# Performance work log

Hardware: AMD Instinct MI355X
Metric: run time of the kernel (lower is better)

Reference implementation:

```python
import jax, jax.numpy as jnp
import numpy as np

V, D, H, L, T, B = 50257, 768, 12, 12, 1024, 2
S = 0.02


def setup_inputs() -> dict:
    key = jax.random.key(0)
    ks = jax.random.split(key, 8)
    return {
        "idx": jax.random.randint(ks[0], (B, T), 0, V),
        "wte": jax.random.normal(ks[1], (V, D), jnp.float32) * S,   # tied tok_emb / head
        "pos": jax.random.normal(ks[2], (T, D), jnp.float32) * S,
        "ln1_g": jnp.ones((L, D), jnp.float32),
        "ln1_b": jnp.zeros((L, D), jnp.float32),
        "qkv_w": jax.random.normal(ks[3], (L, D, 3 * D), jnp.float32) * S,
        "qkv_b": jnp.zeros((L, 3 * D), jnp.float32),
        "proj_w": jax.random.normal(ks[4], (L, D, D), jnp.float32) * S,
        "proj_b": jnp.zeros((L, D), jnp.float32),
        "ln2_g": jnp.ones((L, D), jnp.float32),
        "ln2_b": jnp.zeros((L, D), jnp.float32),
        "fc1_w": jax.random.normal(ks[5], (L, D, 4 * D), jnp.float32) * S,
        "fc1_b": jnp.zeros((L, 4 * D), jnp.float32),
        "fc2_w": jax.random.normal(ks[6], (L, 4 * D, D), jnp.float32) * S,
        "fc2_b": jnp.zeros((L, D), jnp.float32),
        "lnf_g": jnp.ones((D,), jnp.float32),
        "lnf_b": jnp.zeros((D,), jnp.float32),
    }


def _ln(x, g, b):
    m = x.mean(-1, keepdims=True)
    v = ((x - m) ** 2).mean(-1, keepdims=True)
    return (x - m) * jax.lax.rsqrt(v + 1e-5) * g + b


def reference(idx, wte, pos, ln1_g, ln1_b, qkv_w, qkv_b, proj_w, proj_b,
              ln2_g, ln2_b, fc1_w, fc1_b, fc2_w, fc2_b, lnf_g, lnf_b):
    b, t = idx.shape
    hd = D // H
    x = wte[idx] + pos[None, :t]                       # [B,T,D]
    causal = jnp.triu(jnp.ones((t, t), bool), 1)       # True above diagonal -> masked

    def block(x, p):
        l1g, l1b, qw, qb, pw, pb, l2g, l2b, f1w, f1b, f2w, f2b = p
        h = _ln(x, l1g, l1b)
        qkv = (h @ qw + qb).reshape(b, t, 3, H, hd).transpose(2, 0, 3, 1, 4)
        q, k, v = qkv[0], qkv[1], qkv[2]               # [B,H,T,hd]
        att = jnp.einsum('bhqd,bhkd->bhqk', q, k) * hd ** -0.5
        att = jnp.where(causal, -jnp.inf, att)
        att = jax.nn.softmax(att, axis=-1)
        o = jnp.einsum('bhqk,bhkd->bhqd', att, v)
        o = o.transpose(0, 2, 1, 3).reshape(b, t, D)
        x = x + o @ pw + pb
        h = _ln(x, l2g, l2b)
        h = jax.nn.gelu(h @ f1w + f1b, approximate=False)
        x = x + h @ f2w + f2b
        return x, None

    x, _ = jax.lax.scan(block, x, (ln1_g, ln1_b, qkv_w, qkv_b, proj_w, proj_b,
                                   ln2_g, ln2_b, fc1_w, fc1_b, fc2_w, fc2_b))
    x = _ln(x, lnf_g, lnf_b)
    return x @ wte.T                                   # tied head -> [B,T,V]
```

## Files before the change

### kernel.cpp

```cpp
#include <hip/hip_runtime.h>
#include <math.h>

#define D 768
#define T 1024
#define BATCH 2
#define NH 12
#define NL 12
#define V 50257
#define NT 2048

typedef _Float16 half4_t __attribute__((ext_vector_type(4)));
typedef _Float16 half8_t __attribute__((ext_vector_type(8)));
typedef float floatx4 __attribute__((ext_vector_type(4)));

__device__ inline float wave_reduce_sum(float v) {
  #pragma unroll
  for (int off = 32; off > 0; off >>= 1) v += __shfl_xor(v, off, 64);
  return v;
}

__device__ __forceinline__ void gld16(const _Float16* g, _Float16* l) {
  __builtin_amdgcn_global_load_lds(
      (const __attribute__((address_space(1))) unsigned int*)g,
      (__attribute__((address_space(3))) unsigned int*)l, 16, 0, 0);
}

__global__ __launch_bounds__(256) void embed_kernel(const int* __restrict__ idx,
    const float* __restrict__ wte, const float* __restrict__ pos,
    float* __restrict__ x) {
  int row = blockIdx.x;
  int tok = idx[row];
  int tp  = row & (T - 1);
  const float* ws = wte + (size_t)tok * D;
  const float* ps = pos + (size_t)tp * D;
  float* xr = x + (size_t)row * D;
  for (int i = threadIdx.x; i < D; i += 256) xr[i] = ws[i] + ps[i];
}

__global__ __launch_bounds__(256) void cvt16_kernel(const float* __restrict__ src,
    _Float16* __restrict__ dst, int n4) {
  int i = blockIdx.x * 256 + threadIdx.x;
  int stride = gridDim.x * 256;
  for (; i < n4; i += stride) {
    float4 v = ((const float4*)src)[i];
    half4_t h;
    h[0] = (_Float16)v.x; h[1] = (_Float16)v.y;
    h[2] = (_Float16)v.z; h[3] = (_Float16)v.w;
    ((half4_t*)dst)[i] = h;
  }
}

__global__ __launch_bounds__(256) void wconv_kernel(
    const float* __restrict__ qkvw, const float* __restrict__ projw,
    const float* __restrict__ fc1w, const float* __restrict__ fc2w,
    _Float16* __restrict__ q16, _Float16* __restrict__ p16,
    _Float16* __restrict__ f116, _Float16* __restrict__ f216) {
  int id = blockIdx.x;
  size_t l = blockIdx.y;
  const float* src; _Float16* dst; int K, N, tn;
  if (id < 1728)      { src = qkvw + l * (D * 3 * D); dst = q16  + l * (2304 * 768); K = 768;  N = 2304; tn = id; }
  else if (id < 2304) { src = projw + l * (D * D);    dst = p16  + l * (768 * 768);  K = 768;  N = 768;  tn = id - 1728; }
  else if (id < 4608) { src = fc1w + l * (D * 4 * D); dst = f116 + l * (3072 * 768); K = 768;  N = 3072; tn = id - 2304; }
  else                { src = fc2w + l * (4 * D * D); dst = f216 + l * (3072 * 768); K = 3072; N = 768;  tn = id - 4608; }
  int ntn = N >> 5;
  int tc = (tn % ntn) * 32;
  int tr = (tn / ntn) * 32;
  __shared__ float tile[32][33];
  int tx = threadIdx.x & 31, ty = threadIdx.x >> 5;
  #pragma unroll
  for (int j = 0; j < 4; ++j)
    tile[ty + 8 * j][tx] = src[(size_t)(tr + ty + 8 * j) * N + tc + tx];
  __syncthreads();
  #pragma unroll
  for (int j = 0; j < 4; ++j)
    dst[(size_t)(tc + ty + 8 * j) * K + tr + tx] = (_Float16)tile[tx][ty + 8 * j];
}

__global__ __launch_bounds__(256) void ln_kernel(const float* __restrict__ x,
    const float* __restrict__ g, const float* __restrict__ bta,
    _Float16* __restrict__ y) {
  const int lane = threadIdx.x & 63, wave = threadIdx.x >> 6;
  const int row = blockIdx.x * 4 + wave;
  const float4* xr = (const float4*)(x + (size_t)row * D);
  half4_t* yr = (half4_t*)(y + (size_t)row * D);

  float4 a[3];
  #pragma unroll
  for (int j = 0; j < 3; ++j) a[j] = xr[lane + 64 * j];

  float s = 0.f;
  #pragma unroll
  for (int j = 0; j < 3; ++j) s += a[j].x + a[j].y + a[j].z + a[j].w;
  float mean = wave_reduce_sum(s) * (1.f / D);

  float v = 0.f;
  #pragma unroll
  for (int j = 0; j < 3; ++j) {
    float dx = a[j].x - mean, dy = a[j].y - mean, dz = a[j].z - mean, dw = a[j].w - mean;
    v += dx * dx + dy * dy + dz * dz + dw * dw;
  }
  float rstd = rsqrtf(wave_reduce_sum(v) * (1.f / D) + 1e-5f);

  #pragma unroll
  for (int j = 0; j < 3; ++j) {
    float4 gg = ((const float4*)g)[lane + 64 * j];
    float4 bb = ((const float4*)bta)[lane + 64 * j];
    half4_t h;
    h[0] = (_Float16)((a[j].x - mean) * rstd * gg.x + bb.x);
    h[1] = (_Float16)((a[j].y - mean) * rstd * gg.y + bb.y);
    h[2] = (_Float16)((a[j].z - mean) * rstd * gg.z + bb.z);
    h[3] = (_Float16)((a[j].w - mean) * rstd * gg.w + bb.w);
    yr[lane + 64 * j] = h;
  }
}

__global__ __launch_bounds__(256) void attn_kernel(
    const _Float16* __restrict__ qkv,
    const _Float16* __restrict__ vt,
    _Float16* __restrict__ o) {
  const int qt   = (int)gridDim.x - 1 - (int)blockIdx.x;
  const int h    = blockIdx.y;
  const int b    = blockIdx.z;
  const int tid  = threadIdx.x;
  const int lane = tid & 63, wave = tid >> 6;
  const int lr = lane & 15, g = lane >> 4;
  const int lk = g * 8;
  const int cr = g * 4;

  __shared__ __align__(16) _Float16 Ks[2][64][32];
  __shared__ __align__(16) _Float16 Vs[2][64][32];
  __shared__ __align__(16) _Float16 Pl[4][16][72];

  const int RS = 3 * D;
  const int q0 = qt * 64 + wave * 16;

  const _Float16* qrow = qkv + (size_t)(b * T + q0 + lr) * RS + h * 64;
  half8_t aq0 = *(const half8_t*)(qrow + lk);
  half8_t aq1 = *(const half8_t*)(qrow + 32 + lk);
  #pragma unroll
  for (int j = 0; j < 8; ++j) { aq0[j] *= (_Float16)0.125f; aq1[j] *= (_Float16)0.125f; }

  const int sr = wave * 16 + (lane >> 2);
  const int sc = (lane & 3) * 8;
  const _Float16* ksrc = qkv + (size_t)(b * T + sr) * RS + D + h * 64 + sc;
  const _Float16* vsrc = vt + (size_t)((b * NH + h) * 64 + sr) * T + sc;
  _Float16* kdst0 = &Ks[0][wave * 16][0];
  _Float16* kdst1 = &Ks[1][wave * 16][0];
  _Float16* vdst0 = &Vs[0][wave * 16][0];
  _Float16* vdst1 = &Vs[1][wave * 16][0];

  floatx4 oa[4] = {};
  float m_r[4] = {-1e30f, -1e30f, -1e30f, -1e30f};
  float l_r[4] = {0.f, 0.f, 0.f, 0.f};

  for (int kt = 0; kt <= qt; ++kt) {
    const _Float16* kp = ksrc + (size_t)(kt * 64) * RS;
    gld16(kp, kdst0);
    gld16(kp + 32, kdst1);
    gld16(vsrc + kt * 64, vdst0);
    gld16(vsrc + kt * 64 + 32, vdst1);
    __syncthreads();

    floatx4 s4[4];
    #pragma unroll
    for (int kc = 0; kc < 4; ++kc) {
      half8_t bk0 = *(const half8_t*)&Ks[0][kc * 16 + lr][lk];
      half8_t bk1 = *(const half8_t*)&Ks[1][kc * 16 + lr][lk];
      floatx4 z = {};
      z = __builtin_amdgcn_mfma_f32_16x16x32_f16(aq0, bk0, z, 0, 0, 0);
      z = __builtin_amdgcn_mfma_f32_16x16x32_f16(aq1, bk1, z, 0, 0, 0);
      s4[kc] = z;
    }
    if (kt == qt) {
      #pragma unroll
      for (int kc = 0; kc < 4; ++kc)
        #pragma unroll
        for (int i = 0; i < 4; ++i)
          if (kc * 16 + lr > wave * 16 + cr + i) s4[kc][i] = -1e30f;
    }

    float alpha[4], psum[4];
    #pragma unroll
    for (int i = 0; i < 4; ++i) {
      float v = fmaxf(fmaxf(s4[0][i], s4[1][i]), fmaxf(s4[2][i], s4[3][i]));
      #pragma unroll
      for (int off = 1; off < 16; off <<= 1) v = fmaxf(v, __shfl_xor(v, off, 64));
      float mn = fmaxf(m_r[i], v);
      alpha[i] = __expf(m_r[i] - mn);
      m_r[i] = mn;
      psum[i] = 0.f;
    }
    #pragma unroll
    for (int kc = 0; kc < 4; ++kc)
      #pragma unroll
      for (int i = 0; i < 4; ++i) {
        float p = __expf(s4[kc][i] - m_r[i]);
        psum[i] += p;
        Pl[wave][cr + i][kc * 16 + lr] = (_Float16)p;
      }
    #pragma unroll
    for (int i = 0; i < 4; ++i) {
      float s = psum[i];
      #pragma unroll
      for (int off = 1; off < 16; off <<= 1) s += __shfl_xor(s, off, 64);
      l_r[i] = l_r[i] * alpha[i] + s;
    }
    #pragma unroll
    for (int dc = 0; dc < 4; ++dc)
      #pragma unroll
      for (int i = 0; i < 4; ++i) oa[dc][i] *= alpha[i];

    half8_t ap0 = *(const half8_t*)&Pl[wave][lr][lk];
    half8_t ap1 = *(const half8_t*)&Pl[wave][lr][32 + lk];
    #pragma unroll
    for (int dc = 0; dc < 4; ++dc) {
      half8_t bv0 = *(const half8_t*)&Vs[0][dc * 16 + lr][lk];
      half8_t bv1 = *(const half8_t*)&Vs[1][dc * 16 + lr][lk];
      oa[dc] = __builtin_amdgcn_mfma_f32_16x16x32_f16(ap0, bv0, oa[dc], 0, 0, 0);
      oa[dc] = __builtin_amdgcn_mfma_f32_16x16x32_f16(ap1, bv1, oa[dc], 0, 0, 0);
    }
    __syncthreads();
  }

  _Float16* orow = o + (size_t)(b * T + q0) * D + h * 64;
  #pragma unroll
  for (int i = 0; i < 4; ++i) {
    float inv = 1.f / l_r[i];
    #pragma unroll
    for (int dc = 0; dc < 4; ++dc)
      orow[(size_t)(cr + i) * D + dc * 16 + lr] = (_Float16)(oa[dc][i] * inv);
  }
}

template <bool GELU, bool VT, bool ATOMIC, typename OutT>
__global__ __launch_bounds__(256) void gemm16_kernel(
    const _Float16* __restrict__ A, const _Float16* __restrict__ Bt,
    const float* __restrict__ bias, const float* __restrict__ res,
    OutT* __restrict__ C, _Float16* __restrict__ vt, int M, int N, int K) {
  __shared__ __align__(16) _Float16 As[128][32];
  __shared__ __align__(16) _Float16 Bs[128][32];
  const int t = threadIdx.x;
  const int lane = t & 63, wave = t >> 6;

  const int gx = gridDim.x, gy = gridDim.y;
  const int nwg = gx * gy;
  int f = blockIdx.y * gx + blockIdx.x;
  int id = (f & 7) * (nwg >> 3) + (f >> 3);
  const int n0 = (id / gy) * 128;
  const int m0 = (id % gy) * 128;

  const int ks = K / gridDim.z;
  const int kbeg = blockIdx.z * ks, kend = kbeg + ks;

  const int wm = (wave >> 1) * 64, wn = (wave & 1) * 64;
  const int lr = lane & 15;
  const int lk = (lane >> 4) * 8;

  const int srow = lane >> 2;
  const int scol = (lane & 3) * 8;
  const _Float16* a_src0 = A + (size_t)(m0 + wave * 32 + srow) * K + scol;
  const _Float16* a_src1 = a_src0 + (size_t)16 * K;
  const int bn0 = min(n0 + wave * 32 + srow, N - 1);
  const int bn1 = min(n0 + wave * 32 + 16 + srow, N - 1);
  const _Float16* b_src0 = Bt + (size_t)bn0 * K + scol;
  const _Float16* b_src1 = Bt + (size_t)bn1 * K + scol;
  _Float16* a_dst0 = &As[wave * 32][0];
  _Float16* a_dst1 = &As[wave * 32 + 16][0];
  _Float16* b_dst0 = &Bs[wave * 32][0];
  _Float16* b_dst1 = &Bs[wave * 32 + 16][0];

  floatx4 acc[4][4] = {};

  for (int k0 = kbeg; k0 < kend; k0 += 32) {
    gld16(a_src0 + k0, a_dst0);
    gld16(a_src1 + k0, a_dst1);
    gld16(b_src0 + k0, b_dst0);
    gld16(b_src1 + k0, b_dst1);
    __syncthreads();

    half8_t af[4], bf[4];
    #pragma unroll
    for (int mi = 0; mi < 4; ++mi)
      af[mi] = *(const half8_t*)&As[wm + mi * 16 + lr][lk];
    #pragma unroll
    for (int ni = 0; ni < 4; ++ni)
      bf[ni] = *(const half8_t*)&Bs[wn + ni * 16 + lr][lk];
    #pragma unroll
    for (int mi = 0; mi < 4; ++mi)
      #pragma unroll
      for (int ni = 0; ni < 4; ++ni)
        acc[mi][ni] = __builtin_amdgcn_mfma_f32_16x16x32_f16(
            af[mi], bf[ni], acc[mi][ni], 0, 0, 0);
    __syncthreads();
  }

  const int cr = (lane >> 4) * 4;
  #pragma unroll
  for (int mi = 0; mi < 4; ++mi) {
    #pragma unroll
    for (int ni = 0; ni < 4; ++ni) {
      int n = n0 + wn + ni * 16 + lr;
      if (n >= N) continue;
      floatx4 v = acc[mi][ni];
      float bs = (bias && (!ATOMIC || blockIdx.z == 0)) ? bias[n] : 0.f;
      if (VT && n >= 2 * D) {
        int d  = n - 2 * D;
        int mb = m0 + wm + mi * 16 + cr;
        half4_t h4;
        #pragma unroll
        for (int i = 0; i < 4; ++i) h4[i] = (_Float16)(v[i] + bs);
        *(half4_t*)(vt + ((size_t)((mb >> 10) * NH + (d >> 6)) * 64 + (d & 63)) * T
                       + (mb & 1023)) = h4;
      } else if (ATOMIC) {
        #pragma unroll
        for (int i = 0; i < 4; ++i) {
          int m = m0 + wm + mi * 16 + cr + i;
          atomicAdd((float*)&C[(size_t)m * N + n], v[i] + bs);
        }
      } else {
        #pragma unroll
        for (int i = 0; i < 4; ++i) {
          int m = m0 + wm + mi * 16 + cr + i;
          float vv = v[i] + bs;
          if (res)  vv += res[(size_t)m * N + n];
          if (GELU) vv = 0.5f * vv * (1.f + erff(vv * 0.70710678118f));
          C[(size_t)m * N + n] = (OutT)vv;
        }
      }
    }
  }
}

extern "C" void kernel_launch(void* const* d_in, const int* in_sizes, int n_in,
                              void* d_out, int out_size, void* d_ws, size_t ws_size,
                              hipStream_t stream) {
  const int*   idx   = (const int*)d_in[0];
  const float* wte   = (const float*)d_in[1];
  const float* pos   = (const float*)d_in[2];
  const float* ln1g  = (const float*)d_in[3];
  const float* ln1b  = (const float*)d_in[4];
  const float* qkvw  = (const float*)d_in[5];
  const float* qkvb  = (const float*)d_in[6];
  const float* projw = (const float*)d_in[7];
  const float* projb = (const float*)d_in[8];
  const float* ln2g  = (const float*)d_in[9];
  const float* ln2b  = (const float*)d_in[10];
  const float* fc1w  = (const float*)d_in[11];
  const float* fc1b  = (const float*)d_in[12];
  const float* fc2w  = (const float*)d_in[13];
  const float* fc2b  = (const float*)d_in[14];
  const float* lnfg  = (const float*)d_in[15];
  const float* lnfb  = (const float*)d_in[16];
  float* out = (float*)d_out;

  float* ws = (float*)d_ws;
  float* x = ws;
  _Float16* big16  = (_Float16*)(x + (size_t)NT * D);
  _Float16* vt16   = big16 + (size_t)NT * 4 * D;
  _Float16* hbuf16 = vt16 + (size_t)BATCH * NH * 64 * T;
  _Float16* obuf16 = hbuf16 + (size_t)NT * D;
  _Float16* wte16  = obuf16 + (size_t)NT * D;
  _Float16* wbase  = wte16 + (size_t)V * D;

  const size_t QSZ = (size_t)2304 * 768, PSZ = (size_t)768 * 768;
  const size_t F1SZ = (size_t)3072 * 768, F2SZ = (size_t)3072 * 768;
  const size_t PERL = QSZ + PSZ + F1SZ + F2SZ;
  const size_t fixed_bytes = (char*)wbase - (char*)d_ws;
  const bool all12 = ws_size >= fixed_bytes + 12 * PERL * sizeof(_Float16);
  const int nlw = all12 ? 12 : 1;

  _Float16* q16  = wbase;
  _Float16* p16  = q16  + QSZ * nlw;
  _Float16* f116 = p16  + PSZ * nlw;
  _Float16* f216 = f116 + F1SZ * nlw;

  cvt16_kernel<<<2048, 256, 0, stream>>>(wte, wte16, (V * D) / 4);
  embed_kernel<<<NT, 256, 0, stream>>>(idx, wte, pos, x);
  if (all12)
    wconv_kernel<<<dim3(6912, 12), 256, 0, stream>>>(
        qkvw, projw, fc1w, fc2w, q16, p16, f116, f216);

  for (int l = 0; l < NL; ++l) {
    size_t lw = all12 ? (size_t)l : 0;
    if (!all12)
      wconv_kernel<<<dim3(6912, 1), 256, 0, stream>>>(
          qkvw + (size_t)l * D * 3 * D, projw + (size_t)l * D * D,
          fc1w + (size_t)l * D * 4 * D, fc2w + (size_t)l * 4 * D * D,
          q16, p16, f116, f216);
    ln_kernel<<<NT / 4, 256, 0, stream>>>(x, ln1g + (size_t)l * D, ln1b + (size_t)l * D, hbuf16);
    gemm16_kernel<false, true, false, _Float16><<<dim3(18, 16), 256, 0, stream>>>(
        hbuf16, q16 + lw * QSZ, qkvb + (size_t)l * 3 * D, nullptr, big16, vt16, NT, 3 * D, D);
    attn_kernel<<<dim3(T / 64, NH, BATCH), 256, 0, stream>>>(big16, vt16, obuf16);
    gemm16_kernel<false, false, true, float><<<dim3(6, 16, 2), 256, 0, stream>>>(
        obuf16, p16 + lw * PSZ, projb + (size_t)l * D, nullptr, x, nullptr, NT, D, D);
    ln_kernel<<<NT / 4, 256, 0, stream>>>(x, ln2g + (size_t)l * D, ln2b + (size_t)l * D, hbuf16);
    gemm16_kernel<true, false, false, _Float16><<<dim3(24, 16), 256, 0, stream>>>(
        hbuf16, f116 + lw * F1SZ, fc1b + (size_t)l * 4 * D, nullptr, big16, nullptr, NT, 4 * D, D);
    gemm16_kernel<false, false, true, float><<<dim3(6, 16, 4), 256, 0, stream>>>(
        big16, f216 + lw * F2SZ, fc2b + (size_t)l * D, nullptr, x, nullptr, NT, D, 4 * D);
  }

  ln_kernel<<<NT / 4, 256, 0, stream>>>(x, lnfg, lnfb, hbuf16);
  gemm16_kernel<false, false, false, float><<<dim3((V + 127) / 128, 16), 256, 0, stream>>>(
      hbuf16, wte16, nullptr, nullptr, out, nullptr, NT, V, D);
}
```

Before: 3.072 ms.

## Double-buffer LDS tiles in attention and GEMM, nontemporal logits stores

Both the attention kernel and the generic GEMM kernel now keep two LDS buffers and issue the global-to-LDS loads for the next K tile before computing on the current one. This is meant to overlap memory latency with MFMA work. It doubles LDS usage per block, which may lower occupancy. The final vocabulary-projection GEMM also writes its large fp32 logits output with nontemporal stores to avoid polluting the cache.

```diff
diff --git a/kernel.cpp b/kernel.cpp
--- a/kernel.cpp
+++ b/kernel.cpp
@@ -127,8 +127,8 @@
   const int lk = g * 8;
   const int cr = g * 4;
 
-  __shared__ __align__(16) _Float16 Ks[2][64][32];
-  __shared__ __align__(16) _Float16 Vs[2][64][32];
+  __shared__ __align__(16) _Float16 Ks[2][2][64][32];
+  __shared__ __align__(16) _Float16 Vs[2][2][64][32];
   __shared__ __align__(16) _Float16 Pl[4][16][72];
 
   const int RS = 3 * D;
@@ -144,28 +144,31 @@
   const int sc = (lane & 3) * 8;
   const _Float16* ksrc = qkv + (size_t)(b * T + sr) * RS + D + h * 64 + sc;
   const _Float16* vsrc = vt + (size_t)((b * NH + h) * 64 + sr) * T + sc;
-  _Float16* kdst0 = &Ks[0][wave * 16][0];
-  _Float16* kdst1 = &Ks[1][wave * 16][0];
-  _Float16* vdst0 = &Vs[0][wave * 16][0];
-  _Float16* vdst1 = &Vs[1][wave * 16][0];
+
+#define ASTAGE(bufn, kk) do {                                   \
+    const _Float16* kp_ = ksrc + (size_t)((kk) * 64) * RS;      \
+    gld16(kp_,      &Ks[bufn][0][wave * 16][0]);                \
+    gld16(kp_ + 32, &Ks[bufn][1][wave * 16][0]);                \
+    gld16(vsrc + (kk) * 64,      &Vs[bufn][0][wave * 16][0]);   \
+    gld16(vsrc + (kk) * 64 + 32, &Vs[bufn][1][wave * 16][0]);   \
+  } while (0)
 
   floatx4 oa[4] = {};
   float m_r[4] = {-1e30f, -1e30f, -1e30f, -1e30f};
   float l_r[4] = {0.f, 0.f, 0.f, 0.f};
 
+  ASTAGE(0, 0);
+  __syncthreads();
+
   for (int kt = 0; kt <= qt; ++kt) {
-    const _Float16* kp = ksrc + (size_t)(kt * 64) * RS;
-    gld16(kp, kdst0);
-    gld16(kp + 32, kdst1);
-    gld16(vsrc + kt * 64, vdst0);
-    gld16(vsrc + kt * 64 + 32, vdst1);
-    __syncthreads();
+    const int cur = kt & 1;
+    if (kt < qt) ASTAGE(cur ^ 1, kt + 1);
 
     floatx4 s4[4];
     #pragma unroll
     for (int kc = 0; kc < 4; ++kc) {
-      half8_t bk0 = *(const half8_t*)&Ks[0][kc * 16 + lr][lk];
-      half8_t bk1 = *(const half8_t*)&Ks[1][kc * 16 + lr][lk];
+      half8_t bk0 = *(const half8_t*)&Ks[cur][0][kc * 16 + lr][lk];
+      half8_t bk1 = *(const half8_t*)&Ks[cur][1][kc * 16 + lr][lk];
       floatx4 z = {};
       z = __builtin_amdgcn_mfma_f32_16x16x32_f16(aq0, bk0, z, 0, 0, 0);
       z = __builtin_amdgcn_mfma_f32_16x16x32_f16(aq1, bk1, z, 0, 0, 0);
@@ -214,13 +217,14 @@
     half8_t ap1 = *(const half8_t*)&Pl[wave][lr][32 + lk];
     #pragma unroll
     for (int dc = 0; dc < 4; ++dc) {
-      half8_t bv0 = *(const half8_t*)&Vs[0][dc * 16 + lr][lk];
-      half8_t bv1 = *(const half8_t*)&Vs[1][dc * 16 + lr][lk];
+      half8_t bv0 = *(const half8_t*)&Vs[cur][0][dc * 16 + lr][lk];
+      half8_t bv1 = *(const half8_t*)&Vs[cur][1][dc * 16 + lr][lk];
       oa[dc] = __builtin_amdgcn_mfma_f32_16x16x32_f16(ap0, bv0, oa[dc], 0, 0, 0);
       oa[dc] = __builtin_amdgcn_mfma_f32_16x16x32_f16(ap1, bv1, oa[dc], 0, 0, 0);
     }
     __syncthreads();
   }
+#undef ASTAGE
 
   _Float16* orow = o + (size_t)(b * T + q0) * D + h * 64;
   #pragma unroll
@@ -232,13 +236,13 @@
   }
 }
 
-template <bool GELU, bool VT, bool ATOMIC, typename OutT>
+template <bool GELU, bool VT, bool ATOMIC, bool NTS, typename OutT>
 __global__ __launch_bounds__(256) void gemm16_kernel(
     const _Float16* __restrict__ A, const _Float16* __restrict__ Bt,
     const float* __restrict__ bias, const float* __restrict__ res,
     OutT* __restrict__ C, _Float16* __restrict__ vt, int M, int N, int K) {
-  __shared__ __align__(16) _Float16 As[128][32];
-  __shared__ __align__(16) _Float16 Bs[128][32];
+  __shared__ __align__(16) _Float16 As[2][128][32];
+  __shared__ __align__(16) _Float16 Bs[2][128][32];
   const int t = threadIdx.x;
   const int lane = t & 63, wave = t >> 6;
 
@@ -264,35 +268,40 @@
   const int bn1 = min(n0 + wave * 32 + 16 + srow, N - 1);
   const _Float16* b_src0 = Bt + (size_t)bn0 * K + scol;
   const _Float16* b_src1 = Bt + (size_t)bn1 * K + scol;
-  _Float16* a_dst0 = &As[wave * 32][0];
-  _Float16* a_dst1 = &As[wave * 32 + 16][0];
-  _Float16* b_dst0 = &Bs[wave * 32][0];
-  _Float16* b_dst1 = &Bs[wave * 32 + 16][0];
+
+#define GSTAGE(bufn, kk) do {                            \
+    gld16(a_src0 + (kk), &As[bufn][wave * 32][0]);       \
+    gld16(a_src1 + (kk), &As[bufn][wave * 32 + 16][0]);  \
+    gld16(b_src0 + (kk), &Bs[bufn][wave * 32][0]);       \
+    gld16(b_src1 + (kk), &Bs[bufn][wave * 32 + 16][0]);  \
+  } while (0)
 
   floatx4 acc[4][4] = {};
 
-  for (int k0 = kbeg; k0 < kend; k0 += 32) {
-    gld16(a_src0 + k0, a_dst0);
-    gld16(a_src1 + k0, a_dst1);
-    gld16(b_src0 + k0, b_dst0);
-    gld16(b_src1 + k0, b_dst1);
-    __syncthreads();
-
-    half8_t af[4], bf[4];
+  GSTAGE(0, kbeg);
+  __syncthreads();
+
+  const int nIter = (kend - kbeg) >> 5;
+  for (int i = 0; i < nIter; ++i) {
+    const int cur = i & 1;
+    if (i + 1 < nIter) GSTAGE(cur ^ 1, kbeg + ((i + 1) << 5));
+
+    half8_t af[4], bb[4];
     #pragma unroll
     for (int mi = 0; mi < 4; ++mi)
-      af[mi] = *(const half8_t*)&As[wm + mi * 16 + lr][lk];
+      af[mi] = *(const half8_t*)&As[cur][wm + mi * 16 + lr][lk];
     #pragma unroll
     for (int ni = 0; ni < 4; ++ni)
-      bf[ni] = *(const half8_t*)&Bs[wn + ni * 16 + lr][lk];
+      bb[ni] = *(const half8_t*)&Bs[cur][wn + ni * 16 + lr][lk];
     #pragma unroll
     for (int mi = 0; mi < 4; ++mi)
       #pragma unroll
       for (int ni = 0; ni < 4; ++ni)
         acc[mi][ni] = __builtin_amdgcn_mfma_f32_16x16x32_f16(
-            af[mi], bf[ni], acc[mi][ni], 0, 0, 0);
+            af[mi], bb[ni], acc[mi][ni], 0, 0, 0);
     __syncthreads();
   }
+#undef GSTAGE
 
   const int cr = (lane >> 4) * 4;
   #pragma unroll
@@ -324,7 +333,8 @@
           float vv = v[i] + bs;
           if (res)  vv += res[(size_t)m * N + n];
           if (GELU) vv = 0.5f * vv * (1.f + erff(vv * 0.70710678118f));
-          C[(size_t)m * N + n] = (OutT)vv;
+          if (NTS) __builtin_nontemporal_store((OutT)vv, &C[(size_t)m * N + n]);
+          else     C[(size_t)m * N + n] = (OutT)vv;
         }
       }
     }
@@ -388,19 +398,19 @@
           fc1w + (size_t)l * D * 4 * D, fc2w + (size_t)l * 4 * D * D,
           q16, p16, f116, f216);
     ln_kernel<<<NT / 4, 256, 0, stream>>>(x, ln1g + (size_t)l * D, ln1b + (size_t)l * D, hbuf16);
-    gemm16_kernel<false, true, false, _Float16><<<dim3(18, 16), 256, 0, stream>>>(
+    gemm16_kernel<false, true, false, false, _Float16><<<dim3(18, 16), 256, 0, stream>>>(
         hbuf16, q16 + lw * QSZ, qkvb + (size_t)l * 3 * D, nullptr, big16, vt16, NT, 3 * D, D);
     attn_kernel<<<dim3(T / 64, NH, BATCH), 256, 0, stream>>>(big16, vt16, obuf16);
-    gemm16_kernel<false, false, true, float><<<dim3(6, 16, 2), 256, 0, stream>>>(
+    gemm16_kernel<false, false, true, false, float><<<dim3(6, 16, 2), 256, 0, stream>>>(
         obuf16, p16 + lw * PSZ, projb + (size_t)l * D, nullptr, x, nullptr, NT, D, D);
     ln_kernel<<<NT / 4, 256, 0, stream>>>(x, ln2g + (size_t)l * D, ln2b + (size_t)l * D, hbuf16);
-    gemm16_kernel<true, false, false, _Float16><<<dim3(24, 16), 256, 0, stream>>>(
+    gemm16_kernel<true, false, false, false, _Float16><<<dim3(24, 16), 256, 0, stream>>>(
         hbuf16, f116 + lw * F1SZ, fc1b + (size_t)l * 4 * D, nullptr, big16, nullptr, NT, 4 * D, D);
-    gemm16_kernel<false, false, true, float><<<dim3(6, 16, 4), 256, 0, stream>>>(
+    gemm16_kernel<false, false, true, false, float><<<dim3(6, 16, 4), 256, 0, stream>>>(
         big16, f216 + lw * F2SZ, fc2b + (size_t)l * D, nullptr, x, nullptr, NT, D, 4 * D);
   }
 
   ln_kernel<<<NT / 4, 256, 0, stream>>>(x, lnfg, lnfb, hbuf16);
-  gemm16_kernel<false, false, false, float><<<dim3((V + 127) / 128, 16), 256, 0, stream>>>(
+  gemm16_kernel<false, false, false, true, float><<<dim3((V + 127) / 128, 16), 256, 0, stream>>>(
       hbuf16, wte16, nullptr, nullptr, out, nullptr, NT, V, D);
 }
```

Result: slower. 3.162 ms (+2.9%).
